# Kernel optimization log

Measured on AMD Instinct MI355X. Metric: run time of the kernel, lower is better.

Reference implementation:

```python
import jax, jax.numpy as jnp
import numpy as np

D_MODEL = 768
KERNELS = [7, 5, 3]
FILTERS = [40, 30, 20]
FC_IN = sum(FILTERS)  # 90


def setup_inputs() -> dict:
    key = jax.random.key(0)
    ks = jax.random.split(key, 16)
    B, S, D = 8, 2048, D_MODEL
    inp = {
        'x1': jax.random.normal(ks[0], (B, S, D), jnp.float32),
        'x2': jax.random.normal(ks[1], (B, S, D), jnp.float32),
    }
    # conv weights: OIH layout [out_ch, in_ch, k]
    for i, (k, f) in enumerate(zip(KERNELS, FILTERS)):
        scale = 1.0 / np.sqrt(D * k)
        inp[f'w{k}'] = jax.random.uniform(ks[2 + 2 * i], (f, D, k), jnp.float32, -scale, scale)
        inp[f'b{k}'] = jax.random.uniform(ks[3 + 2 * i], (f,), jnp.float32, -scale, scale)
    inp['U'] = jax.random.normal(ks[8], (D, D), jnp.float32) * (1.0 / np.sqrt(D))
    inp['bias_v'] = jax.random.normal(ks[9], (D,), jnp.float32) * 0.02
    inp['fc_w'] = jax.random.normal(ks[10], (D, FC_IN), jnp.float32) * (1.0 / np.sqrt(FC_IN))
    inp['fc_b'] = jnp.zeros((D,), jnp.float32)
    inp['fcx_w'] = jax.random.normal(ks[11], (D, 2 * D), jnp.float32) * (1.0 / np.sqrt(2 * D))
    inp['fcx_b'] = jnp.zeros((D,), jnp.float32)
    return inp


def _conv1d_same(x_ncs, w_oik, b_o, k):
    # x: [B, C, S], w: [O, C, k] -> [B, O, S], 'same' padding = k//2
    y = jax.lax.conv_general_dilated(
        x_ncs, w_oik, window_strides=(1,), padding=[(k // 2, k // 2)],
        dimension_numbers=('NCH', 'OIH', 'NCH'))
    return y + b_o[None, :, None]


def reference(x1, x2, w7, b7, w5, b5, w3, b3, U, bias_v, fc_w, fc_b, fcx_w, fcx_b):
    # CNN branch over x2 (dropout layers are identity in eval mode)
    xc = jnp.transpose(x2, (0, 2, 1))  # [B, D, S]
    feats = jnp.concatenate([
        jnp.transpose(_conv1d_same(xc, w7, b7, 7), (0, 2, 1)),
        jnp.transpose(_conv1d_same(xc, w5, b5, 5), (0, 2, 1)),
        jnp.transpose(_conv1d_same(xc, w3, b3, 3), (0, 2, 1)),
    ], axis=-1)                                    # [B, S, 90]
    x = jnp.tanh(jax.nn.relu(feats) @ fc_w.T + fc_b)  # [B, S, D]
    # biaffine attention: x1 @ U @ x2^T + x2 @ bias (broadcast over rows)
    attn = jnp.einsum('bsd,de,bte->bst', x1, U, x2) + (x2 @ bias_v)[:, None, :]
    attn = jax.nn.softmax(attn, axis=-1)           # [B, S, S]
    out = jnp.tanh(attn @ x2)                      # [B, S, D]
    x = x + out
    return jnp.concatenate([x1, x], axis=-1) @ fcx_w.T + fcx_b  # [B, S, D]
```

## Files before the change

kernel.cpp:

```cpp
#include <hip/hip_runtime.h>
#include <cmath>

#define D_MODEL 768
#define SEQ 2048
#define BATCH 8
#define FC_PAD 96
#define FC_PAD2 128
#define KCOMB (7 * D_MODEL)
#define KCHUNK 1344

typedef unsigned short ushort_t;
typedef _Float16 half_t;
typedef __attribute__((ext_vector_type(8))) _Float16 f16x8;
typedef __attribute__((ext_vector_type(8))) unsigned short u16x8;
typedef __attribute__((ext_vector_type(4))) unsigned short u16x4;
typedef __attribute__((ext_vector_type(4))) float f32x4;

struct Ptr8 { const ushort_t* p[8]; };

__device__ __forceinline__ ushort_t f2h(float x) {
    half_t h = (half_t)x;
    return __builtin_bit_cast(ushort_t, h);
}
__device__ __forceinline__ float h2f(ushort_t u) {
    return (float)__builtin_bit_cast(half_t, u);
}
__device__ __forceinline__ float fast_tanh(float x) {
    float a = fabsf(x);
    float t = __expf(-2.f * a);
    float r = (1.f - t) / (1.f + t);
    return copysignf(r, x);
}
__device__ __forceinline__ void gload16(const ushort_t* g, ushort_t* lbase) {
    __builtin_amdgcn_global_load_lds((const __attribute__((address_space(1))) void*)g,
                                     (__attribute__((address_space(3))) void*)lbase,
                                     16, 0, 0);
}

__global__ void convert_f16_kernel(const float* __restrict__ src, ushort_t* __restrict__ dst, size_t n4) {
    size_t i = (size_t)blockIdx.x * 256 + threadIdx.x;
    if (i >= n4) return;
    f32x4 x = *(const f32x4*)(src + i * 4);
    u16x4 h;
    #pragma unroll
    for (int j = 0; j < 4; ++j) h[j] = f2h(x[j]);
    *(u16x4*)(dst + i * 4) = h;
}

__global__ void convert_fc_kernel(const float* __restrict__ src, ushort_t* __restrict__ dst) {
    int i = blockIdx.x * 256 + threadIdx.x;
    if (i >= D_MODEL * FC_PAD2) return;
    int o = i / FC_PAD2, j = i - o * FC_PAD2;
    dst[i] = (j < 90) ? f2h(src[o * 90 + j]) : 0;
}

__global__ void convert_ut_kernel(const float* __restrict__ U, ushort_t* __restrict__ dst) {
    int i = blockIdx.x * 256 + threadIdx.x;
    if (i >= D_MODEL * D_MODEL) return;
    int n = i / D_MODEL, k = i - n * D_MODEL;
    dst[i] = f2h(U[(size_t)k * D_MODEL + n]);
}

__global__ void build_wcomb_kernel(const float* __restrict__ w7, const float* __restrict__ b7,
                                   const float* __restrict__ w5, const float* __restrict__ b5,
                                   const float* __restrict__ w3, const float* __restrict__ b3,
                                   ushort_t* __restrict__ Wt, float* __restrict__ bcat) {
    int idx = blockIdx.x * 256 + threadIdx.x;
    const int total = FC_PAD2 * KCOMB;
    if (idx < total) {
        int o = idx / KCOMB, k = idx - o * KCOMB;
        int t = k / D_MODEL, d = k - t * D_MODEL;
        float v = 0.f;
        if (o < 40) {
            v = w7[(size_t)o * (D_MODEL * 7) + d * 7 + t];
        } else if (o < 70) {
            int t5 = t - 1;
            if (t5 >= 0 && t5 < 5) v = w5[(size_t)(o - 40) * (D_MODEL * 5) + d * 5 + t5];
        } else if (o < 90) {
            int t3 = t - 2;
            if (t3 >= 0 && t3 < 3) v = w3[(size_t)(o - 70) * (D_MODEL * 3) + d * 3 + t3];
        }
        Wt[idx] = f2h(v);
    }
    if (idx < FC_PAD2) {
        float bv = 0.f;
        if (idx < 40) bv = b7[idx];
        else if (idx < 70) bv = b5[idx - 40];
        else if (idx < 90) bv = b3[idx - 70];
        bcat[idx] = bv;
    }
}

__global__ void conv_reduce_kernel(const float* __restrict__ P, const float* __restrict__ bcat,
                                   ushort_t* __restrict__ feats) {
    const size_t MT = (size_t)BATCH * SEQ;
    size_t i = (size_t)blockIdx.x * 256 + threadIdx.x;
    if (i >= MT * FC_PAD2) return;
    int col = (int)(i & (FC_PAD2 - 1));
    size_t row = i >> 7;
    float v = 0.f;
    if (col < FC_PAD) {
        size_t idx = row * FC_PAD + col;
        const size_t st = MT * FC_PAD;
        v = P[idx] + P[idx + st] + P[idx + 2 * st] + P[idx + 3 * st] + bcat[col];
        v = fmaxf(v, 0.f);
    }
    feats[i] = f2h(v);
}

__global__ void transpose_f16_kernel(const ushort_t* __restrict__ in, ushort_t* __restrict__ out) {
    __shared__ ushort_t tile[32][40];
    int b = blockIdx.z;
    int s0 = blockIdx.x * 32, d0 = blockIdx.y * 32;
    int tx = threadIdx.x & 31, ty = threadIdx.x >> 5;
    const ushort_t* inb = in + (size_t)b * SEQ * D_MODEL;
    ushort_t* outb = out + (size_t)b * D_MODEL * SEQ;
    #pragma unroll
    for (int i = 0; i < 4; ++i)
        tile[ty + i * 8][tx] = inb[(size_t)(s0 + ty + i * 8) * D_MODEL + d0 + tx];
    __syncthreads();
    #pragma unroll
    for (int i = 0; i < 4; ++i)
        outb[(size_t)(d0 + ty + i * 8) * SEQ + s0 + tx] = tile[tx][ty + i * 8];
}

__global__ void rowbias_kernel(const float* __restrict__ x2, const float* __restrict__ bias_v,
                               float* __restrict__ rowbias) {
    int row = blockIdx.x;
    const float* xr = x2 + (size_t)row * D_MODEL;
    float s = 0.f;
    for (int c = threadIdx.x; c < D_MODEL; c += 256) s += xr[c] * bias_v[c];
    for (int off = 32; off > 0; off >>= 1) s += __shfl_down(s, off);
    __shared__ float red[4];
    int lane = threadIdx.x & 63, w = threadIdx.x >> 6;
    if (lane == 0) red[w] = s;
    __syncthreads();
    if (threadIdx.x == 0) rowbias[row] = red[0] + red[1] + red[2] + red[3];
}

template<int TM, int TN, int AMODE, int ACT, int HASBIAS, int HASADD,
         int OUTMODE, int KSPLIT, int APTR, int MAP, int ZM, int GX, int GY,
         int SMEPI, int ASCALE>
__global__ __launch_bounds__(256, 3)
void mfma_gemm(const ushort_t* __restrict__ A, const ushort_t* __restrict__ A2,
               const ushort_t* __restrict__ B, const float* __restrict__ bias,
               const ushort_t* __restrict__ addsrc,
               float* __restrict__ Cf, ushort_t* __restrict__ Ch,
               Ptr8 ap, float* __restrict__ smw, float* __restrict__ slw,
               int M, int N, int K, int lda, int ldb, int ldc,
               size_t sA, size_t sB, size_t sBias, size_t sC) {
    constexpr int WM = TM / 2, WN = TN / 2, FM = WM / 16, FN = WN / 16;
    __shared__ __align__(16) ushort_t As_[TM * 64];
    __shared__ __align__(16) ushort_t Bs_[TN * 64];
    __shared__ float pmS[SMEPI ? 4 : 1][SMEPI ? 64 : 1];
    __shared__ float msS[SMEPI ? 128 : 1];
    __shared__ float plS[SMEPI ? 4 : 1][SMEPI ? 64 : 1];
    __shared__ float alS[ASCALE ? 16 : 1][ASCALE ? 128 : 1];

    int bx, by, z;
    if (MAP == 1) {
        int lin = blockIdx.x;
        z = lin % ZM;
        int t = lin / ZM;
        bx = t % GX;
        by = t / GX;
    } else if (MAP == 2) {
        int lin = blockIdx.x;
        int xcd = lin & 7;
        int t = lin >> 3;
        by = t % GY;
        bx = xcd * (GX / 8) + t / GY;
        z = 0;
    } else {
        bx = blockIdx.x; by = blockIdx.y; z = blockIdx.z;
    }

    const int kb = KSPLIT ? z * K : 0;
    const ushort_t* Ab = APTR ? ap.p[z] : (A + (KSPLIT ? 0 : (size_t)z * sA));
    const ushort_t* Bb = B + (KSPLIT ? 0 : (size_t)z * sB);
    if (HASBIAS) bias += (size_t)z * sBias;
    if (HASADD) addsrc += (size_t)z * sC;
    if (OUTMODE == 0) Cf += (size_t)z * sC;
    else if (!SMEPI) Ch += (size_t)z * sC;

    const int m0 = bx * TM;
    const int n0 = by * TN;
    const int tid = threadIdx.x;
    const int lane = tid & 63;
    const int wave = tid >> 6;
    const int wm = (wave >> 1) * WM, wn = (wave & 1) * WN;
    const int r16 = lane & 15, kq = lane >> 4;
    const int srow = tid >> 3;
    const int slot = tid & 7;

    if (ASCALE) {
        if (tid < 128) {
            int row = tid;
            int gm = m0 + row;
            float mt[16];
            float mg = -3.0e38f;
            #pragma unroll
            for (int t = 0; t < 16; ++t) {
                mt[t] = smw[((size_t)z * 16 + t) * SEQ + gm];
                mg = fmaxf(mg, mt[t]);
            }
            float lg = 0.f;
            #pragma unroll
            for (int t = 0; t < 16; ++t) {
                float e = __expf(mt[t] - mg);
                lg += slw[((size_t)z * 16 + t) * SEQ + gm] * e;
                alS[t][row] = e;
            }
            float inv = 1.f / lg;
            #pragma unroll
            for (int t = 0; t < 16; ++t) alS[t][row] *= inv;
        }
        __syncthreads();
    }

    f32x4 acc[FM][FN];
    #pragma unroll
    for (int i = 0; i < FM; ++i)
        #pragma unroll
        for (int j = 0; j < FN; ++j) acc[i][j] = (f32x4){0.f, 0.f, 0.f, 0.f};

    const u16x8 zv = {0, 0, 0, 0, 0, 0, 0, 0};

    for (int k0 = 0; k0 < K; k0 += 64) {
        #pragma unroll
        for (int i = 0; i < TM / 32; ++i) {
            int row = i * 32 + srow;
            int gm = m0 + row;
            int xs = slot ^ (row & 7);
            if (AMODE == 1) {
                int gkk = kb + k0 + xs * 8;
                int t = gkk / D_MODEL, d = gkk - t * D_MODEL;
                int s = (gm & (SEQ - 1)) + t - 3;
                int bb = gm >> 11;
                u16x8 v = (s >= 0 && s < SEQ) ? *(const u16x8*)(Ab + ((size_t)(bb * SEQ + s)) * lda + d) : zv;
                *(u16x8*)&As_[(size_t)row * 64 + slot * 8] = v;
            } else {
                const ushort_t* src;
                if (AMODE == 2) {
                    int gk = k0 + xs * 8;
                    src = (gk < D_MODEL) ? Ab + (size_t)gm * D_MODEL + gk
                                         : A2 + (size_t)gm * D_MODEL + (gk - D_MODEL);
                } else {
                    int gk = kb + k0 + xs * 8;
                    src = Ab + (size_t)gm * lda + gk;
                }
                gload16(src, &As_[(size_t)(i * 32 + wave * 8) * 64]);
            }
        }
        #pragma unroll
        for (int i = 0; i < TN / 32; ++i) {
            int row = i * 32 + srow;
            int gn = n0 + row;
            int xs = slot ^ (row & 7);
            int gk = kb + k0 + xs * 8;
            gload16(Bb + (size_t)gn * ldb + gk, &Bs_[(size_t)(i * 32 + wave * 8) * 64]);
        }
        __syncthreads();

        f16x8 ah[FM][2], bh[FN][2];
        #pragma unroll
        for (int mi = 0; mi < FM; ++mi) {
            int row = wm + mi * 16 + r16;
            #pragma unroll
            for (int kk = 0; kk < 2; ++kk)
                ah[mi][kk] = *(const f16x8*)&As_[(size_t)row * 64 + (((kk * 4 + kq) ^ (row & 7)) * 8)];
        }
        if (ASCALE) {
            const int kt = k0 >> 7;
            #pragma unroll
            for (int mi = 0; mi < FM; ++mi) {
                half_t s = (half_t)alS[kt][wm + mi * 16 + r16];
                ah[mi][0] = ah[mi][0] * s;
                ah[mi][1] = ah[mi][1] * s;
            }
        }
        #pragma unroll
        for (int ni = 0; ni < FN; ++ni) {
            int row = wn + ni * 16 + r16;
            #pragma unroll
            for (int kk = 0; kk < 2; ++kk)
                bh[ni][kk] = *(const f16x8*)&Bs_[(size_t)row * 64 + (((kk * 4 + kq) ^ (row & 7)) * 8)];
        }
        #pragma unroll
        for (int kk = 0; kk < 2; ++kk)
            #pragma unroll
            for (int mi = 0; mi < FM; ++mi)
                #pragma unroll
                for (int ni = 0; ni < FN; ++ni)
                    acc[mi][ni] = __builtin_amdgcn_mfma_f32_16x16x32_f16(ah[mi][kk], bh[ni][kk], acc[mi][ni], 0, 0, 0);
        __syncthreads();
    }

    if (SMEPI) {
        float pmax[FM][4];
        #pragma unroll
        for (int mi = 0; mi < FM; ++mi)
            #pragma unroll
            for (int r = 0; r < 4; ++r) {
                float mx = -3.0e38f;
                #pragma unroll
                for (int ni = 0; ni < FN; ++ni) {
                    float v = acc[mi][ni][r] + bias[n0 + wn + ni * 16 + r16];
                    acc[mi][ni][r] = v;
                    mx = fmaxf(mx, v);
                }
                mx = fmaxf(mx, __shfl_xor(mx, 1));
                mx = fmaxf(mx, __shfl_xor(mx, 2));
                mx = fmaxf(mx, __shfl_xor(mx, 4));
                mx = fmaxf(mx, __shfl_xor(mx, 8));
                pmax[mi][r] = mx;
            }
        if (r16 == 0) {
            #pragma unroll
            for (int mi = 0; mi < FM; ++mi)
                #pragma unroll
                for (int r = 0; r < 4; ++r)
                    pmS[wave][mi * 16 + kq * 4 + r] = pmax[mi][r];
        }
        __syncthreads();
        if (tid < 128) {
            int rl = tid & 63, grp = tid >> 6;
            msS[grp * 64 + rl] = fmaxf(pmS[grp * 2][rl], pmS[grp * 2 + 1][rl]);
        }
        __syncthreads();
        #pragma unroll
        for (int mi = 0; mi < FM; ++mi)
            #pragma unroll
            for (int r = 0; r < 4; ++r) {
                float mrow = msS[wm + mi * 16 + kq * 4 + r];
                float s = 0.f;
                #pragma unroll
                for (int ni = 0; ni < FN; ++ni) {
                    float e = __expf(acc[mi][ni][r] - mrow);
                    acc[mi][ni][r] = e;
                    s += e;
                }
                s += __shfl_xor(s, 1);
                s += __shfl_xor(s, 2);
                s += __shfl_xor(s, 4);
                s += __shfl_xor(s, 8);
                pmax[mi][r] = s;
            }
        if (r16 == 0) {
            #pragma unroll
            for (int mi = 0; mi < FM; ++mi)
                #pragma unroll
                for (int r = 0; r < 4; ++r)
                    plS[wave][mi * 16 + kq * 4 + r] = pmax[mi][r];
        }
        __syncthreads();
        if (tid < 128) {
            int rl = tid & 63, grp = tid >> 6;
            int row = grp * 64 + rl;
            float l2 = plS[grp * 2][rl] + plS[grp * 2 + 1][rl];
            size_t si = ((size_t)z * 16 + by) * SEQ + (m0 + row);
            smw[si] = msS[row];
            slw[si] = l2;
        }
        ushort_t* Co = (ushort_t*)ap.p[z];
        #pragma unroll
        for (int mi = 0; mi < FM; ++mi)
            #pragma unroll
            for (int ni = 0; ni < FN; ++ni)
                #pragma unroll
                for (int r = 0; r < 4; ++r) {
                    int gm = m0 + wm + mi * 16 + kq * 4 + r;
                    int gn = n0 + wn + ni * 16 + r16;
                    Co[(size_t)gm * SEQ + gn] = f2h(acc[mi][ni][r]);
                }
        return;
    }

    #pragma unroll
    for (int mi = 0; mi < FM; ++mi)
        #pragma unroll
        for (int ni = 0; ni < FN; ++ni)
            #pragma unroll
            for (int r = 0; r < 4; ++r) {
                int gm = m0 + wm + mi * 16 + kq * 4 + r;
                int gn = n0 + wn + ni * 16 + r16;
                if (gn >= N) continue;
                float v = acc[mi][ni][r];
                if (HASBIAS) v += bias[gn];
                if (ACT == 1) v = fmaxf(v, 0.f);
                else if (ACT == 2) v = fast_tanh(v);
                if (HASADD) v += h2f(addsrc[(size_t)gm * ldc + gn]);
                size_t idx = (size_t)gm * ldc + gn;
                if (OUTMODE == 0) Cf[idx] = v;
                else Ch[idx] = f2h(v);
            }
}

extern "C" void kernel_launch(void* const* d_in, const int* in_sizes, int n_in,
                              void* d_out, int out_size, void* d_ws, size_t ws_size,
                              hipStream_t stream) {
    const float* x1     = (const float*)d_in[0];
    const float* x2     = (const float*)d_in[1];
    const float* w7     = (const float*)d_in[2];
    const float* b7     = (const float*)d_in[3];
    const float* w5     = (const float*)d_in[4];
    const float* b5     = (const float*)d_in[5];
    const float* w3     = (const float*)d_in[6];
    const float* b3     = (const float*)d_in[7];
    const float* U      = (const float*)d_in[8];
    const float* bias_v = (const float*)d_in[9];
    const float* fc_w   = (const float*)d_in[10];
    const float* fc_b   = (const float*)d_in[11];
    const float* fcx_w  = (const float*)d_in[12];
    const float* fcx_b  = (const float*)d_in[13];
    float* out = (float*)d_out;

    const size_t MT = (size_t)BATCH * SEQ;
    const size_t NE = MT * D_MODEL;
    const size_t NEb = (size_t)SEQ * D_MODEL;
    const size_t SEGSZ = (size_t)SEQ * SEQ;

    char* p = (char*)d_ws;
    auto alloc = [&](size_t bytes) -> char* {
        char* r = p;
        p += (bytes + 255) & ~(size_t)255;
        return r;
    };
    ushort_t* x1_h   = (ushort_t*)alloc(NE * 2);
    ushort_t* x2_h   = (ushort_t*)alloc(NE * 2);
    ushort_t* x2t    = (ushort_t*)alloc(NE * 2);
    ushort_t* y1     = (ushort_t*)alloc(NE * 2);
    ushort_t* xcnn   = (ushort_t*)alloc(NE * 2);
    float*    convp  = (float*)   alloc(MT * FC_PAD * 4 * 4);
    ushort_t* feats  = (ushort_t*)alloc(MT * FC_PAD2 * 2);
    ushort_t* Wt     = (ushort_t*)alloc((size_t)FC_PAD2 * KCOMB * 2);
    ushort_t* fc_wt  = (ushort_t*)alloc((size_t)D_MODEL * FC_PAD2 * 2);
    ushort_t* fcx_wt = (ushort_t*)alloc((size_t)D_MODEL * 2 * D_MODEL * 2);
    ushort_t* Ut     = (ushort_t*)alloc((size_t)D_MODEL * D_MODEL * 2);
    float*    bcat   = (float*)alloc(FC_PAD2 * 4);
    float*    rbias  = (float*)alloc(MT * 4);
    float*    smS    = (float*)alloc((size_t)BATCH * 16 * SEQ * 4);
    float*    slS    = (float*)alloc((size_t)BATCH * 16 * SEQ * 4);

    ushort_t* dob = (ushort_t*)d_out;
    Ptr8 ap;
    ap.p[0] = (ushort_t*)convp;
    ap.p[1] = (ushort_t*)convp + SEGSZ;
    ap.p[2] = (ushort_t*)convp + 2 * SEGSZ;
    ap.p[3] = dob;
    ap.p[4] = dob + SEGSZ;
    ap.p[5] = dob + 2 * SEGSZ;
    ap.p[6] = dob + 3 * SEGSZ;
    ap.p[7] = dob + 4 * SEGSZ;
    Ptr8 apz = {};

    const int T = 256;
    auto blk = [](size_t n) { return dim3((unsigned)((n + 255) / 256)); };

    build_wcomb_kernel<<<blk((size_t)FC_PAD2 * KCOMB), T, 0, stream>>>(w7, b7, w5, b5, w3, b3, Wt, bcat);
    convert_fc_kernel<<<blk((size_t)D_MODEL * FC_PAD2), T, 0, stream>>>(fc_w, fc_wt);
    convert_f16_kernel<<<blk((size_t)D_MODEL * 2 * D_MODEL / 4), T, 0, stream>>>(fcx_w, fcx_wt, (size_t)D_MODEL * 2 * D_MODEL / 4);
    convert_ut_kernel<<<blk((size_t)D_MODEL * D_MODEL), T, 0, stream>>>(U, Ut);
    convert_f16_kernel<<<blk(NE / 4), T, 0, stream>>>(x1, x1_h, NE / 4);
    convert_f16_kernel<<<blk(NE / 4), T, 0, stream>>>(x2, x2_h, NE / 4);
    transpose_f16_kernel<<<dim3(SEQ / 32, D_MODEL / 32, BATCH), T, 0, stream>>>(x2_h, x2t);
    rowbias_kernel<<<dim3((unsigned)MT), T, 0, stream>>>(x2, bias_v, rbias);

    mfma_gemm<64, 128, 1, 0, 0, 0, 0, 1, 0, 0, 1, 1, 1, 0, 0><<<dim3(MT / 64, 1, 4), T, 0, stream>>>(
        x2_h, nullptr, Wt, nullptr, nullptr,
        convp, nullptr, apz, nullptr, nullptr,
        (int)MT, FC_PAD, KCHUNK, D_MODEL, KCOMB, FC_PAD,
        0, 0, 0, MT * FC_PAD);
    conv_reduce_kernel<<<blk(MT * FC_PAD2), T, 0, stream>>>(convp, bcat, feats);

    mfma_gemm<128, 128, 0, 2, 1, 0, 1, 0, 0, 2, 1, 128, 6, 0, 0><<<dim3(768, 1, 1), T, 0, stream>>>(
        feats, nullptr, fc_wt, fc_b, nullptr,
        nullptr, xcnn, apz, nullptr, nullptr,
        (int)MT, D_MODEL, FC_PAD2, FC_PAD2, FC_PAD2, D_MODEL, 0, 0, 0, 0);

    mfma_gemm<128, 128, 0, 0, 0, 0, 1, 0, 0, 2, 1, 128, 6, 0, 0><<<dim3(768, 1, 1), T, 0, stream>>>(
        x1_h, nullptr, Ut, nullptr, nullptr,
        nullptr, y1, apz, nullptr, nullptr,
        (int)MT, D_MODEL, D_MODEL, D_MODEL, D_MODEL, D_MODEL, 0, 0, 0, 0);

    mfma_gemm<128, 128, 0, 0, 1, 0, 1, 0, 0, 1, 8, 16, 16, 1, 0><<<dim3(2048, 1, 1), T, 0, stream>>>(
        y1, nullptr, x2_h, rbias, nullptr,
        nullptr, nullptr, ap, smS, slS,
        SEQ, SEQ, D_MODEL, D_MODEL, D_MODEL, SEQ,
        NEb, NEb, SEQ, 0);

    mfma_gemm<128, 128, 0, 2, 0, 1, 1, 0, 1, 1, 8, 16, 6, 0, 1><<<dim3(768, 1, 1), T, 0, stream>>>(
        nullptr, nullptr, x2t, nullptr,
        xcnn,
        nullptr, xcnn, ap, smS, slS,
        SEQ, D_MODEL, SEQ, SEQ, SEQ, D_MODEL,
        0, NEb, 0, NEb);

    mfma_gemm<128, 128, 2, 0, 1, 0, 0, 0, 0, 2, 1, 128, 6, 0, 0><<<dim3(768, 1, 1), T, 0, stream>>>(
        x1_h, xcnn, fcx_wt, fcx_b, nullptr,
        out, nullptr, apz, nullptr, nullptr,
        (int)MT, D_MODEL, 2 * D_MODEL, D_MODEL, 2 * D_MODEL, D_MODEL, 0, 0, 0, 0);
}
```

Baseline: 341.1 us.

## Fold row bias into U GEMM, halve conv split-K, store softmax scales as f16

Removes the separate rowbias kernel by adding bias_v to the x1@U output rows before the score GEMM. Because x1·U·x2ᵀ + 1·(bias·x2ᵀ) = (x1·U + bias)·x2ᵀ, the bias now rides inside the score GEMM. The conv split-K drops from 4 to 2 chunks, which halves the partial-sum traffic in the reduce kernel but leaves fewer blocks. Softmax scale factors are stored as f16 in LDS, and a new block mapping (MAP 3) orders tiles for the PV GEMM. Adding the bias to y1 in f16 adds some rounding risk to the attention scores.

```diff
diff --git a/kernel.cpp b/kernel.cpp
--- a/kernel.cpp
+++ b/kernel.cpp
@@ -7,7 +7,7 @@
 #define FC_PAD 96
 #define FC_PAD2 128
 #define KCOMB (7 * D_MODEL)
-#define KCHUNK 1344
+#define KCHUNK 2688
 
 typedef unsigned short ushort_t;
 typedef _Float16 half_t;
@@ -102,7 +102,7 @@
     if (col < FC_PAD) {
         size_t idx = row * FC_PAD + col;
         const size_t st = MT * FC_PAD;
-        v = P[idx] + P[idx + st] + P[idx + 2 * st] + P[idx + 3 * st] + bcat[col];
+        v = P[idx] + P[idx + st] + bcat[col];
         v = fmaxf(v, 0.f);
     }
     feats[i] = f2h(v);
@@ -122,20 +122,6 @@
     #pragma unroll
     for (int i = 0; i < 4; ++i)
         outb[(size_t)(d0 + ty + i * 8) * SEQ + s0 + tx] = tile[tx][ty + i * 8];
-}
-
-__global__ void rowbias_kernel(const float* __restrict__ x2, const float* __restrict__ bias_v,
-                               float* __restrict__ rowbias) {
-    int row = blockIdx.x;
-    const float* xr = x2 + (size_t)row * D_MODEL;
-    float s = 0.f;
-    for (int c = threadIdx.x; c < D_MODEL; c += 256) s += xr[c] * bias_v[c];
-    for (int off = 32; off > 0; off >>= 1) s += __shfl_down(s, off);
-    __shared__ float red[4];
-    int lane = threadIdx.x & 63, w = threadIdx.x >> 6;
-    if (lane == 0) red[w] = s;
-    __syncthreads();
-    if (threadIdx.x == 0) rowbias[row] = red[0] + red[1] + red[2] + red[3];
 }
 
 template<int TM, int TN, int AMODE, int ACT, int HASBIAS, int HASADD,
@@ -155,7 +141,7 @@
     __shared__ float pmS[SMEPI ? 4 : 1][SMEPI ? 64 : 1];
     __shared__ float msS[SMEPI ? 128 : 1];
     __shared__ float plS[SMEPI ? 4 : 1][SMEPI ? 64 : 1];
-    __shared__ float alS[ASCALE ? 16 : 1][ASCALE ? 128 : 1];
+    __shared__ ushort_t alS[ASCALE ? 16 : 1][ASCALE ? 128 : 1];
 
     int bx, by, z;
     if (MAP == 1) {
@@ -171,6 +157,12 @@
         by = t % GY;
         bx = xcd * (GX / 8) + t / GY;
         z = 0;
+    } else if (MAP == 3) {
+        int lin = blockIdx.x;
+        z = lin % ZM;
+        int t = lin / ZM;
+        by = t % GY;
+        bx = t / GY;
     } else {
         bx = blockIdx.x; by = blockIdx.y; z = blockIdx.z;
     }
@@ -197,7 +189,7 @@
         if (tid < 128) {
             int row = tid;
             int gm = m0 + row;
-            float mt[16];
+            float mt[16], al[16];
             float mg = -3.0e38f;
             #pragma unroll
             for (int t = 0; t < 16; ++t) {
@@ -209,11 +201,11 @@
             for (int t = 0; t < 16; ++t) {
                 float e = __expf(mt[t] - mg);
                 lg += slw[((size_t)z * 16 + t) * SEQ + gm] * e;
-                alS[t][row] = e;
+                al[t] = e;
             }
             float inv = 1.f / lg;
             #pragma unroll
-            for (int t = 0; t < 16; ++t) alS[t][row] *= inv;
+            for (int t = 0; t < 16; ++t) alS[t][row] = f2h(al[t] * inv);
         }
         __syncthreads();
     }
@@ -274,7 +266,7 @@
             const int kt = k0 >> 7;
             #pragma unroll
             for (int mi = 0; mi < FM; ++mi) {
-                half_t s = (half_t)alS[kt][wm + mi * 16 + r16];
+                half_t s = __builtin_bit_cast(half_t, alS[kt][wm + mi * 16 + r16]);
                 ah[mi][0] = ah[mi][0] * s;
                 ah[mi][1] = ah[mi][1] * s;
             }
@@ -305,8 +297,8 @@
                 float mx = -3.0e38f;
                 #pragma unroll
                 for (int ni = 0; ni < FN; ++ni) {
-                    float v = acc[mi][ni][r] + bias[n0 + wn + ni * 16 + r16];
-                    acc[mi][ni][r] = v;
+                    float v = acc[mi][ni][r];
+                    if (HASBIAS) { v += bias[n0 + wn + ni * 16 + r16]; acc[mi][ni][r] = v; }
                     mx = fmaxf(mx, v);
                 }
                 mx = fmaxf(mx, __shfl_xor(mx, 1));
@@ -438,7 +430,6 @@
     ushort_t* fcx_wt = (ushort_t*)alloc((size_t)D_MODEL * 2 * D_MODEL * 2);
     ushort_t* Ut     = (ushort_t*)alloc((size_t)D_MODEL * D_MODEL * 2);
     float*    bcat   = (float*)alloc(FC_PAD2 * 4);
-    float*    rbias  = (float*)alloc(MT * 4);
     float*    smS    = (float*)alloc((size_t)BATCH * 16 * SEQ * 4);
     float*    slS    = (float*)alloc((size_t)BATCH * 16 * SEQ * 4);
 
@@ -464,9 +455,8 @@
     convert_f16_kernel<<<blk(NE / 4), T, 0, stream>>>(x1, x1_h, NE / 4);
     convert_f16_kernel<<<blk(NE / 4), T, 0, stream>>>(x2, x2_h, NE / 4);
     transpose_f16_kernel<<<dim3(SEQ / 32, D_MODEL / 32, BATCH), T, 0, stream>>>(x2_h, x2t);
-    rowbias_kernel<<<dim3((unsigned)MT), T, 0, stream>>>(x2, bias_v, rbias);
-
-    mfma_gemm<64, 128, 1, 0, 0, 0, 0, 1, 0, 0, 1, 1, 1, 0, 0><<<dim3(MT / 64, 1, 4), T, 0, stream>>>(
+
+    mfma_gemm<64, 128, 1, 0, 0, 0, 0, 1, 0, 0, 1, 1, 1, 0, 0><<<dim3(MT / 64, 1, 2), T, 0, stream>>>(
         x2_h, nullptr, Wt, nullptr, nullptr,
         convp, nullptr, apz, nullptr, nullptr,
         (int)MT, FC_PAD, KCHUNK, D_MODEL, KCOMB, FC_PAD,
@@ -478,18 +468,18 @@
         nullptr, xcnn, apz, nullptr, nullptr,
         (int)MT, D_MODEL, FC_PAD2, FC_PAD2, FC_PAD2, D_MODEL, 0, 0, 0, 0);
 
-    mfma_gemm<128, 128, 0, 0, 0, 0, 1, 0, 0, 2, 1, 128, 6, 0, 0><<<dim3(768, 1, 1), T, 0, stream>>>(
-        x1_h, nullptr, Ut, nullptr, nullptr,
+    mfma_gemm<128, 128, 0, 0, 1, 0, 1, 0, 0, 2, 1, 128, 6, 0, 0><<<dim3(768, 1, 1), T, 0, stream>>>(
+        x1_h, nullptr, Ut, bias_v, nullptr,
         nullptr, y1, apz, nullptr, nullptr,
         (int)MT, D_MODEL, D_MODEL, D_MODEL, D_MODEL, D_MODEL, 0, 0, 0, 0);
 
-    mfma_gemm<128, 128, 0, 0, 1, 0, 1, 0, 0, 1, 8, 16, 16, 1, 0><<<dim3(2048, 1, 1), T, 0, stream>>>(
-        y1, nullptr, x2_h, rbias, nullptr,
+    mfma_gemm<128, 128, 0, 0, 0, 0, 1, 0, 0, 1, 8, 16, 16, 1, 0><<<dim3(2048, 1, 1), T, 0, stream>>>(
+        y1, nullptr, x2_h, nullptr, nullptr,
         nullptr, nullptr, ap, smS, slS,
         SEQ, SEQ, D_MODEL, D_MODEL, D_MODEL, SEQ,
-        NEb, NEb, SEQ, 0);
-
-    mfma_gemm<128, 128, 0, 2, 0, 1, 1, 0, 1, 1, 8, 16, 6, 0, 1><<<dim3(768, 1, 1), T, 0, stream>>>(
+        NEb, NEb, 0, 0);
+
+    mfma_gemm<128, 128, 0, 2, 0, 1, 1, 0, 1, 3, 8, 16, 6, 0, 1><<<dim3(768, 1, 1), T, 0, stream>>>(
         nullptr, nullptr, x2t, nullptr,
         xcnn,
         nullptr, xcnn, ap, smS, slS,
```

Result: no change. 340.0 us (-0.3%).
